# Kernel optimization log

Hardware: AMD Instinct MI355X
Metric: run time of the kernel (lower is better)

## Reference

```python
import jax, jax.numpy as jnp
import numpy as np
import math

B, T, C, H, D = 2, 2048, 768, 12, 64


def _rms_norm(x):
    # torch F.rms_norm with eps=None -> finfo(dtype).eps, no learned weight
    eps = jnp.finfo(x.dtype).eps
    return x * jax.lax.rsqrt(jnp.mean(x * x, axis=-1, keepdims=True) + eps)


def _apply_rotary(x, cos, sin):
    # nanochat rotary: split head_dim into halves
    d = x.shape[-1] // 2
    x1, x2 = x[..., :d], x[..., d:]
    return jnp.concatenate([x1 * cos + x2 * sin, -x1 * sin + x2 * cos], axis=-1)


def setup_inputs() -> dict:
    key = jax.random.key(0)
    ks = jax.random.split(key, 8)
    s = 0.02
    x = jax.random.normal(ks[0], (B, T, C), jnp.float32)
    cos = jax.random.normal(ks[1], (1, T, 1, D // 2), jnp.float32)
    sin = jax.random.normal(ks[2], (1, T, 1, D // 2), jnp.float32)
    Wq = jax.random.normal(ks[3], (C, C), jnp.float32) * s
    Wk = jax.random.normal(ks[4], (C, C), jnp.float32) * s
    Wv = jax.random.normal(ks[5], (C, C), jnp.float32) * s
    Wo = jax.random.normal(ks[6], (C, C), jnp.float32) * s
    beta = jnp.ones((H,), jnp.float32) * 0.5
    return {"x": x, "cos": cos, "sin": sin, "Wq": Wq, "Wk": Wk, "Wv": Wv, "Wo": Wo, "beta": beta}


def reference(x, cos, sin, Wq, Wk, Wv, Wo, beta):
    b, t, c = x.shape
    h = beta.shape[0]
    d = c // h
    q = (x @ Wq.T).reshape(b, t, h, d)
    k = (x @ Wk.T).reshape(b, t, h, d)
    v = (x @ Wv.T).reshape(b, t, h, d)
    q = _rms_norm(_apply_rotary(q, cos, sin)).transpose(0, 2, 1, 3)  # (B,H,T,D)
    k = _rms_norm(_apply_rotary(k, cos, sin)).transpose(0, 2, 1, 3)
    v = v.transpose(0, 2, 1, 3)
    # phase coherence: mean over RoPE frequencies of cos(position_diff * theta)
    pos = jnp.arange(t, dtype=jnp.float32)
    theta = 10000.0 ** (-jnp.arange(0, d, 2, dtype=jnp.float32) / d)  # (D/2,)
    pdiff = pos[None, :] - pos[:, None]  # (T,T); cos is even so orientation is irrelevant
    coh_base = jnp.mean(jnp.cos(pdiff[:, :, None] * theta), axis=-1)  # (T,T)
    coherence = 1.0 + beta[None, :, None, None] * coh_base[None, None, :, :]  # (1,H,T,T)
    scores = jnp.einsum('bhqd,bhkd->bhqk', q, k) / math.sqrt(d)
    scores = scores * coherence
    w = jax.nn.softmax(scores, axis=-1)
    causal = jnp.tril(jnp.ones((t, t), dtype=bool))
    w = w * causal[None, None, :, :]
    w = w / (jnp.sum(w, axis=-1, keepdims=True) + 1e-8)
    y = jnp.einsum('bhqk,bhkd->bhqd', w, v)
    y = y.transpose(0, 2, 1, 3).reshape(b, t, c)
    return y @ Wo.T
```

## Files before the change

kernel.cpp:

```cpp
#include <hip/hip_runtime.h>
#include <hip/hip_bf16.h>
#include <math.h>

#define B_ 2
#define T_ 2048
#define C_ 768
#define H_ 12
#define D_ 64

typedef __attribute__((ext_vector_type(8))) short short8;
typedef __attribute__((ext_vector_type(4))) float f32x4;
typedef __attribute__((ext_vector_type(16))) float f32x16;

template <bool V> struct BoolC { static constexpr bool value = V; };

#define SBAR() do { asm volatile("" ::: "memory"); __builtin_amdgcn_s_barrier(); asm volatile("" ::: "memory"); } while (0)
#define WAITVM(N) asm volatile("s_waitcnt vmcnt(" #N ")" ::: "memory")

__device__ inline unsigned short f2bf(float f) {
    unsigned int x = __float_as_uint(f);
    unsigned int r = x + 0x7FFFu + ((x >> 16) & 1u);
    return (unsigned short)(r >> 16);
}

__device__ __forceinline__ unsigned cvtpk(float lo, float hi) {
    unsigned r;
    asm("v_cvt_pk_bf16_f32 %0, %1, %2" : "=v"(r) : "v"(lo), "v"(hi));
    return r;
}

__device__ __forceinline__ void plswap(unsigned& a, unsigned& b) {
    asm volatile("v_permlane32_swap_b32 %0, %1" : "+v"(a), "+v"(b));
}

__device__ __forceinline__ void gll16(const void* g, void* l) {
    __builtin_amdgcn_global_load_lds(
        (const __attribute__((address_space(1))) unsigned int*)g,
        (__attribute__((address_space(3))) unsigned int*)l, 16, 0, 0);
}

__global__ __launch_bounds__(256) void convert_all_kernel(const float* __restrict__ x,
                                                          const float* __restrict__ Wq,
                                                          const float* __restrict__ Wk,
                                                          const float* __restrict__ Wv,
                                                          const float* __restrict__ Wo,
                                                          unsigned short* __restrict__ xb,
                                                          unsigned short* __restrict__ wqkv,
                                                          unsigned short* __restrict__ wob,
                                                          float* __restrict__ coh) {
    if (blockIdx.x >= 5376) {
        int dd = (blockIdx.x - 5376) * 256 + threadIdx.x;
        if (dd < T_) {
            float s = 0.f;
            for (int m = 0; m < 32; ++m) {
                float theta = powf(10000.f, -(float)m / 32.f);
                s += cosf((float)dd * theta);
            }
            coh[dd] = s * (1.f / 32.f);
        }
        return;
    }
    int i = blockIdx.x * 256 + threadIdx.x;
    float4 v;
    ushort4* d;
    if (i < 786432) {
        v = ((const float4*)x)[i];
        d = (ushort4*)xb + i;
    } else {
        int wI = i - 786432;
        int widx = wI / 147456;
        int off = wI - widx * 147456;
        const float* W = widx == 0 ? Wq : widx == 1 ? Wk : widx == 2 ? Wv : Wo;
        v = ((const float4*)W)[off];
        unsigned short* base = (widx == 3) ? wob : (wqkv + widx * 589824);
        d = (ushort4*)base + off;
    }
    ushort4 o;
    o.x = f2bf(v.x); o.y = f2bf(v.y); o.z = f2bf(v.z); o.w = f2bf(v.w);
    *d = o;
}

union QkvSmem {
    struct { unsigned short A[3][128][32]; unsigned short Bm[3][64][32]; } g;
    unsigned short tr[64][136];
};

__global__ __launch_bounds__(256, 4) void gemm_qkv_kernel(const unsigned short* __restrict__ xb,
                                                          const unsigned short* __restrict__ wqkv,
                                                          const float* __restrict__ cosb,
                                                          const float* __restrict__ sinb,
                                                          unsigned short* __restrict__ qbf,
                                                          unsigned short* __restrict__ kbf,
                                                          unsigned short* __restrict__ vt) {
    __shared__ QkvSmem sm;

    int bm = blockIdx.x, tn = blockIdx.y;
    int tid = threadIdx.x;
    int w = tid >> 6, lane = tid & 63;
    int rc = lane & 15, kg = lane >> 4;

    const unsigned short* ga = xb + (size_t)(bm * 128 + w * 32 + (lane >> 2)) * 768 + (lane & 3) * 8;
    const unsigned short* gb = wqkv + (size_t)(tn * 64 + w * 16 + (lane >> 2)) * 768 + (lane & 3) * 8;

    f32x4 acc[2][4];
    #pragma unroll
    for (int i = 0; i < 2; ++i)
        #pragma unroll
        for (int j = 0; j < 4; ++j) acc[i][j] = (f32x4){0.f, 0.f, 0.f, 0.f};

    auto stageg = [&](int buf, int k0) {
        gll16(ga + k0, &sm.g.A[buf][w * 32][0]);
        gll16(ga + k0 + 16 * 768, &sm.g.A[buf][w * 32 + 16][0]);
        gll16(gb + k0, &sm.g.Bm[buf][w * 16][0]);
    };
    auto comp = [&](int buf) {
        short8 aF[2], bF[4];
        #pragma unroll
        for (int ai = 0; ai < 2; ++ai) aF[ai] = *(const short8*)&sm.g.A[buf][w * 32 + ai * 16 + rc][kg * 8];
        #pragma unroll
        for (int bj = 0; bj < 4; ++bj) bF[bj] = *(const short8*)&sm.g.Bm[buf][bj * 16 + rc][kg * 8];
        __builtin_amdgcn_s_setprio(1);
        #pragma unroll
        for (int ai = 0; ai < 2; ++ai)
            #pragma unroll
            for (int bj = 0; bj < 4; ++bj)
                acc[ai][bj] = __builtin_amdgcn_mfma_f32_16x16x32_bf16(aF[ai], bF[bj], acc[ai][bj], 0, 0, 0);
        __builtin_amdgcn_s_setprio(0);
    };

    stageg(0, 0);
    stageg(1, 32);
    __syncthreads();
    for (int kk = 0; kk < 22; ++kk) {
        stageg((kk + 2) % 3, (kk + 2) * 32);
        WAITVM(6);
        SBAR();
        comp(kk % 3);
        SBAR();
    }
    WAITVM(3);
    SBAR();
    comp(1);
    SBAR();
    WAITVM(0);
    SBAR();
    comp(2);
    __syncthreads();

    int tensor = tn / 12;
    int h = tn % 12;

    if (tensor < 2) {
        float scale = tensor == 0 ? 0.125f : 1.0f;
        unsigned short* dst = (tensor == 0 ? qbf : kbf);
        #pragma unroll
        for (int ai = 0; ai < 2; ++ai) {
            #pragma unroll
            for (int rr = 0; rr < 4; ++rr) {
                int m = bm * 128 + w * 32 + ai * 16 + kg * 4 + rr;
                int b = m >> 11, t = m & 2047;
                float c0 = cosb[t * 32 + rc], c1 = cosb[t * 32 + 16 + rc];
                float s0 = sinb[t * 32 + rc], s1 = sinb[t * 32 + 16 + rc];
                float x0 = acc[ai][0][rr], x1 = acc[ai][1][rr];
                float x2 = acc[ai][2][rr], x3 = acc[ai][3][rr];
                float o0 = x0 * c0 + x2 * s0;
                float o1 = x1 * c1 + x3 * s1;
                float o2 = -x0 * s0 + x2 * c0;
                float o3 = -x1 * s1 + x3 * c1;
                float ss = o0 * o0 + o1 * o1 + o2 * o2 + o3 * o3;
                ss += __shfl_xor(ss, 1); ss += __shfl_xor(ss, 2);
                ss += __shfl_xor(ss, 4); ss += __shfl_xor(ss, 8);
                float rn = rsqrtf(ss * (1.f / 64.f) + 1.1920929e-07f) * scale;
                unsigned short* dp = dst + (((size_t)b * H_ + h) * T_ + t) * 64;
                dp[rc]      = f2bf(o0 * rn);
                dp[16 + rc] = f2bf(o1 * rn);
                dp[32 + rc] = f2bf(o2 * rn);
                dp[48 + rc] = f2bf(o3 * rn);
            }
        }
    } else {
        #pragma unroll
        for (int ai = 0; ai < 2; ++ai)
            #pragma unroll
            for (int bj = 0; bj < 4; ++bj)
                #pragma unroll
                for (int rr = 0; rr < 4; ++rr)
                    sm.tr[bj * 16 + rc][w * 32 + ai * 16 + kg * 4 + rr] = f2bf(acc[ai][bj][rr]);
        __syncthreads();
        int m0 = bm * 128;
        int b = m0 >> 11, t0 = m0 & 2047;
        int d = w * 16 + (lane >> 2);
        int tl = (lane & 3) * 32;
        unsigned short* gp = vt + (((size_t)b * H_ + h) * 64 + d) * T_ + t0 + tl;
        #pragma unroll
        for (int i = 0; i < 4; ++i)
            *(uint4*)(gp + i * 8) = *(const uint4*)&sm.tr[d][tl + i * 8];
    }
}

__global__ __launch_bounds__(256, 4) void gemm_out_kernel(const unsigned short* __restrict__ A,
                                                          const unsigned short* __restrict__ Bw,
                                                          float* __restrict__ C) {
    __shared__ unsigned short lA[2][64][32];
    __shared__ unsigned short lB[2][64][32];
    int bm = blockIdx.x, tn = blockIdx.y;
    int tid = threadIdx.x;
    int w = tid >> 6, lane = tid & 63;
    int rc = lane & 15, kg = lane >> 4;
    int wr = w >> 1, wc = w & 1;

    const unsigned short* ga = A + (size_t)(bm * 64 + w * 16 + (lane >> 2)) * 768 + (lane & 3) * 8;
    const unsigned short* gbB = Bw + (size_t)(tn * 64 + w * 16 + (lane >> 2)) * 768 + (lane & 3) * 8;

    f32x4 acc[2][2];
    #pragma unroll
    for (int i = 0; i < 2; ++i)
        #pragma unroll
        for (int j = 0; j < 2; ++j) acc[i][j] = (f32x4){0.f, 0.f, 0.f, 0.f};

    auto stageg = [&](int buf, int k0) {
        gll16(ga + k0, &lA[buf][w * 16][0]);
        gll16(gbB + k0, &lB[buf][w * 16][0]);
    };
    auto comp = [&](int buf) {
        short8 aF[2], bF[2];
        #pragma unroll
        for (int ai = 0; ai < 2; ++ai) aF[ai] = *(const short8*)&lA[buf][wr * 32 + ai * 16 + rc][kg * 8];
        #pragma unroll
        for (int bj = 0; bj < 2; ++bj) bF[bj] = *(const short8*)&lB[buf][wc * 32 + bj * 16 + rc][kg * 8];
        __builtin_amdgcn_s_setprio(1);
        #pragma unroll
        for (int ai = 0; ai < 2; ++ai)
            #pragma unroll
            for (int bj = 0; bj < 2; ++bj)
                acc[ai][bj] = __builtin_amdgcn_mfma_f32_16x16x32_bf16(aF[ai], bF[bj], acc[ai][bj], 0, 0, 0);
        __builtin_amdgcn_s_setprio(0);
    };

    stageg(0, 0);
    __syncthreads();
    for (int kk = 0; kk < 23; ++kk) {
        stageg((kk + 1) & 1, (kk + 1) * 32);
        WAITVM(2);
        SBAR();
        comp(kk & 1);
        SBAR();
    }
    WAITVM(0);
    SBAR();
    comp(1);

    #pragma unroll
    for (int ai = 0; ai < 2; ++ai)
        #pragma unroll
        for (int rr = 0; rr < 4; ++rr) {
            int m = bm * 64 + wr * 32 + ai * 16 + kg * 4 + rr;
            #pragma unroll
            for (int bj = 0; bj < 2; ++bj)
                C[(size_t)m * 768 + tn * 64 + wc * 32 + bj * 16 + rc] = acc[ai][bj][rr];
        }
}

__global__ __launch_bounds__(256, 4) void attn_flash_kernel(const unsigned short* __restrict__ qbf,
                                                            const unsigned short* __restrict__ kbf,
                                                            const unsigned short* __restrict__ vt,
                                                            const float* __restrict__ coh,
                                                            const float* __restrict__ beta,
                                                            unsigned short* __restrict__ yb) {
    __shared__ unsigned short kT[2][64][64];
    __shared__ unsigned short vT[2][64][64];
    __shared__ float cfl[T_];

    int p = blockIdx.x;
    int xcd = p & 7, kk = p >> 3;
    int bl = kk >> 5, c = kk & 31;
    int bh = xcd * 3 + bl;
    int tq;
    if (bl == 0)      tq = c;
    else if (bl == 1) tq = (c & 1) ? (15 - (c >> 1)) : (31 - (c >> 1));
    else              tq = (c & 1) ? (31 - (c >> 1)) : (15 - (c >> 1));
    int b = bh / H_, h = bh % H_;

    int tid = threadIdx.x;
    int w = tid >> 6, lane = tid & 63;
    int qs = w >> 1, js = w & 1;
    int ql = lane & 31, hl = lane >> 5;

    float bv = beta[h];
    int cmax4 = (tq + 1) * 16;
    for (int i = tid; i < cmax4; i += 256) {
        float4 cv = ((const float4*)coh)[i];
        float4 o;
        o.x = (1.f + bv * cv.x) * 1.4426950408889634f;
        o.y = (1.f + bv * cv.y) * 1.4426950408889634f;
        o.z = (1.f + bv * cv.z) * 1.4426950408889634f;
        o.w = (1.f + bv * cv.w) * 1.4426950408889634f;
        *(float4*)&cfl[i * 4] = o;
    }

    int qb = tq * 64;
    const unsigned short* kb = kbf + (size_t)bh * T_ * 64;
    const unsigned short* vb = vt + (size_t)bh * 64 * T_;

    const unsigned short* qrow = qbf + ((size_t)bh * T_ + qb + qs * 32 + ql) * 64 + hl * 8;
    short8 qf[4];
    #pragma unroll
    for (int d = 0; d < 4; ++d) qf[d] = *(const short8*)(qrow + d * 16);

    f32x16 acc0, acc1;
    #pragma unroll
    for (int i = 0; i < 16; ++i) { acc0[i] = 0.f; acc1[i] = 0.f; }
    float z = 0.f;

    int Rk = js * 32 + ql;
    int kby[4];
    #pragma unroll
    for (int d = 0; d < 4; ++d) kby[d] = Rk * 128 + (((d * 2 + hl) ^ (Rk & 7)) << 4);
    int vby0[2], vby1[2];
    #pragma unroll
    for (int ks = 0; ks < 2; ++ks) {
        int Rv0 = ql, Rv1 = 32 + ql;
        vby0[ks] = Rv0 * 128 + (((js * 4 + ks * 2 + hl) ^ (Rv0 & 7)) << 4);
        vby1[ks] = Rv1 * 128 + (((js * 4 + ks * 2 + hl) ^ (Rv1 & 7)) << 4);
    }
    const char* kbase = (const char*)&kT[0][0][0];
    const char* vbase = (const char*)&vT[0][0][0];

    int rloc = lane >> 3;
    int gsw = ((lane & 7) ^ rloc) * 8;
    int r0 = w * 16;

    auto stage = [&](int buf, int tj) {
        gll16(kb + (size_t)(tj + r0 + rloc) * 64 + gsw,      &kT[buf][r0][0]);
        gll16(kb + (size_t)(tj + r0 + 8 + rloc) * 64 + gsw,  &kT[buf][r0 + 8][0]);
        gll16(vb + (size_t)(r0 + rloc) * T_ + tj + gsw,      &vT[buf][r0][0]);
        gll16(vb + (size_t)(r0 + 8 + rloc) * T_ + tj + gsw,  &vT[buf][r0 + 8][0]);
    };

    int qpos = qb + qs * 32 + ql;

    auto body = [&](int buf, int tj, auto maskc) {
        constexpr bool M = decltype(maskc)::value;
        f32x16 s;
        #pragma unroll
        for (int i = 0; i < 16; ++i) s[i] = 0.f;
        const char* kp = kbase + buf * 8192;
        __builtin_amdgcn_s_setprio(1);
        #pragma unroll
        for (int d = 0; d < 4; ++d) {
            short8 kf = *(const short8*)(kp + kby[d]);
            s = __builtin_amdgcn_mfma_f32_32x32x16_bf16(kf, qf[d], s, 0, 0, 0);
        }
        __builtin_amdgcn_s_setprio(0);
        int base = qpos - tj - js * 32 - 4 * hl;
        float e[16];
        #pragma unroll
        for (int r = 0; r < 16; ++r) {
            int dd = base - ((r & 3) + 8 * (r >> 2));
            if constexpr (M) {
                float ex = __builtin_amdgcn_exp2f(s[r] * cfl[dd < 0 ? 0 : dd]);
                e[r] = dd >= 0 ? ex : 0.f;
            } else {
                e[r] = __builtin_amdgcn_exp2f(s[r] * cfl[dd]);
            }
            z += e[r];
        }
        unsigned A0 = cvtpk(e[0], e[1]),  B0 = cvtpk(e[2], e[3]);
        unsigned C0 = cvtpk(e[4], e[5]),  D0 = cvtpk(e[6], e[7]);
        unsigned E0 = cvtpk(e[8], e[9]),  F0 = cvtpk(e[10], e[11]);
        unsigned G0 = cvtpk(e[12], e[13]), H0 = cvtpk(e[14], e[15]);
        plswap(A0, C0); plswap(B0, D0); plswap(E0, G0); plswap(F0, H0);
        union U { unsigned u[4]; short8 s8; };
        U p0, p1;
        p0.u[0] = A0; p0.u[1] = B0; p0.u[2] = C0; p0.u[3] = D0;
        p1.u[0] = E0; p1.u[1] = F0; p1.u[2] = G0; p1.u[3] = H0;
        const char* vp = vbase + buf * 8192;
        short8 v00 = *(const short8*)(vp + vby0[0]);
        short8 v01 = *(const short8*)(vp + vby0[1]);
        short8 v10 = *(const short8*)(vp + vby1[0]);
        short8 v11 = *(const short8*)(vp + vby1[1]);
        __builtin_amdgcn_s_setprio(1);
        acc0 = __builtin_amdgcn_mfma_f32_32x32x16_bf16(v00, p0.s8, acc0, 0, 0, 0);
        acc0 = __builtin_amdgcn_mfma_f32_32x32x16_bf16(v01, p1.s8, acc0, 0, 0, 0);
        acc1 = __builtin_amdgcn_mfma_f32_32x32x16_bf16(v10, p0.s8, acc1, 0, 0, 0);
        acc1 = __builtin_amdgcn_mfma_f32_32x32x16_bf16(v11, p1.s8, acc1, 0, 0, 0);
        __builtin_amdgcn_s_setprio(0);
    };

    int nt = tq + 1;
    stage(0, 0);
    __syncthreads();
    int cur = 0;
    for (int it = 0; it < nt - 1; ++it) {
        stage(cur ^ 1, (it + 1) * 64);
        WAITVM(4);
        SBAR();
        body(cur, it * 64, BoolC<false>{});
        SBAR();
        cur ^= 1;
    }
    WAITVM(0);
    SBAR();
    if (qs > js)      body(cur, (nt - 1) * 64, BoolC<false>{});
    else if (qs == js) body(cur, (nt - 1) * 64, BoolC<true>{});
    __syncthreads();

    z += __shfl_xor(z, 32);
    float* osc = (float*)&kT[0][0][0];
    float* zbuf = (float*)&vT[0][0][0];
    if (js == 0) {
        float* o = osc + qs * 2048;
        #pragma unroll
        for (int r = 0; r < 16; ++r) {
            o[r * 64 + lane] = acc0[r];
            o[(16 + r) * 64 + lane] = acc1[r];
        }
        if (lane < 32) zbuf[qs * 32 + ql] = z;
    }
    __syncthreads();
    if (js == 1) {
        float zt = z + zbuf[qs * 32 + ql];
        float invz = 1.f / zt;
        const float* o = osc + qs * 2048;
        #pragma unroll
        for (int r = 0; r < 16; ++r) {
            acc0[r] = (acc0[r] + o[r * 64 + lane]) * invz;
            acc1[r] = (acc1[r] + o[(16 + r) * 64 + lane]) * invz;
        }
        int t = qb + qs * 32 + ql;
        unsigned short* yp = yb + (((size_t)b * T_ + t) * H_ + h) * 64;
        #pragma unroll
        for (int g = 0; g < 4; ++g) {
            uint2 st0, st1;
            st0.x = cvtpk(acc0[g * 4 + 0], acc0[g * 4 + 1]);
            st0.y = cvtpk(acc0[g * 4 + 2], acc0[g * 4 + 3]);
            *(uint2*)(yp + g * 8 + 4 * hl) = st0;
            st1.x = cvtpk(acc1[g * 4 + 0], acc1[g * 4 + 1]);
            st1.y = cvtpk(acc1[g * 4 + 2], acc1[g * 4 + 3]);
            *(uint2*)(yp + 32 + g * 8 + 4 * hl) = st1;
        }
    }
}

extern "C" void kernel_launch(void* const* d_in, const int* in_sizes, int n_in,
                              void* d_out, int out_size, void* d_ws, size_t ws_size,
                              hipStream_t stream) {
    const float* x    = (const float*)d_in[0];
    const float* cosb = (const float*)d_in[1];
    const float* sinb = (const float*)d_in[2];
    const float* Wq   = (const float*)d_in[3];
    const float* Wk   = (const float*)d_in[4];
    const float* Wv   = (const float*)d_in[5];
    const float* Wo   = (const float*)d_in[6];
    const float* beta = (const float*)d_in[7];
    float* out = (float*)d_out;

    char* ws = (char*)d_ws;
    unsigned short* xb   = (unsigned short*)(ws + 0);
    unsigned short* wqkv = (unsigned short*)(ws + 6291456);
    unsigned short* wob  = (unsigned short*)(ws + 9830400);
    unsigned short* qbf  = (unsigned short*)(ws + 11010048);
    unsigned short* kbf  = (unsigned short*)(ws + 17301504);
    unsigned short* vt   = (unsigned short*)(ws + 23592960);
    unsigned short* yb   = (unsigned short*)(ws + 29884416);
    float*          coh  = (float*)(ws + 36175872);

    convert_all_kernel<<<5384, 256, 0, stream>>>(x, Wq, Wk, Wv, Wo, xb, wqkv, wob, coh);

    dim3 gq(32, 36);
    gemm_qkv_kernel<<<gq, 256, 0, stream>>>(xb, wqkv, cosb, sinb, qbf, kbf, vt);

    attn_flash_kernel<<<B_ * H_ * (T_ / 64), 256, 0, stream>>>(qbf, kbf, vt, coh, beta, yb);

    dim3 go(64, 12);
    gemm_out_kernel<<<go, 256, 0, stream>>>(yb, wob, out);
}
```

Measured before the change: 97.64 us.

## Split long causal query tiles across two KV-range blocks with combine kernel

Query tiles 16-31 now have their key range split into two halves, each handled by a separate block that writes unnormalized partial outputs and softmax denominators to workspace. A new combine kernel sums the partials, normalizes, and writes bf16 output. The grid grows from 768 to 1152 blocks to even out the causal work imbalance and shorten the critical path. The cost is an extra launch plus fp32 partial traffic through global memory, and the combine kernel writes scattered 2-byte stores.

```diff
diff --git a/kernel.cpp b/kernel.cpp
--- a/kernel.cpp
+++ b/kernel.cpp
@@ -266,19 +266,29 @@
                                                             const unsigned short* __restrict__ vt,
                                                             const float* __restrict__ coh,
                                                             const float* __restrict__ beta,
-                                                            unsigned short* __restrict__ yb) {
+                                                            unsigned short* __restrict__ yb,
+                                                            float* __restrict__ po,
+                                                            float* __restrict__ pz) {
     __shared__ unsigned short kT[2][64][64];
     __shared__ unsigned short vT[2][64][64];
     __shared__ float cfl[T_];
 
     int p = blockIdx.x;
     int xcd = p & 7, kk = p >> 3;
-    int bl = kk >> 5, c = kk & 31;
+    int bl = kk / 48, u = kk % 48;
     int bh = xcd * 3 + bl;
-    int tq;
-    if (bl == 0)      tq = c;
-    else if (bl == 1) tq = (c & 1) ? (15 - (c >> 1)) : (31 - (c >> 1));
-    else              tq = (c & 1) ? (31 - (c >> 1)) : (15 - (c >> 1));
+    int tq, ts, te, part;
+    if (u < 16) { tq = u; ts = 0; te = tq + 1; part = 0; }
+    else {
+        int idx = u - 16;
+        tq = 16 + (idx >> 1);
+        part = idx & 1;
+        int ht = (tq + 1) >> 1;
+        ts = part ? ht : 0;
+        te = part ? (tq + 1) : ht;
+    }
+    bool hasdiag = (te == tq + 1);
+    bool partial = (u >= 16);
     int b = bh / H_, h = bh % H_;
 
     int tid = threadIdx.x;
@@ -286,9 +296,13 @@
     int qs = w >> 1, js = w & 1;
     int ql = lane & 31, hl = lane >> 5;
 
+    int qb = tq * 64;
     float bv = beta[h];
-    int cmax4 = (tq + 1) * 16;
-    for (int i = tid; i < cmax4; i += 256) {
+    int f0 = qb - te * 64 + 1;
+    if (f0 < 0) f0 = 0;
+    f0 >>= 2;
+    int f1 = (qb + 63 - ts * 64) >> 2;
+    for (int i = f0 + tid; i <= f1; i += 256) {
         float4 cv = ((const float4*)coh)[i];
         float4 o;
         o.x = (1.f + bv * cv.x) * 1.4426950408889634f;
@@ -298,7 +312,6 @@
         *(float4*)&cfl[i * 4] = o;
     }
 
-    int qb = tq * 64;
     const unsigned short* kb = kbf + (size_t)bh * T_ * 64;
     const unsigned short* vb = vt + (size_t)bh * 64 * T_;
 
@@ -387,11 +400,10 @@
         __builtin_amdgcn_s_setprio(0);
     };
 
-    int nt = tq + 1;
-    stage(0, 0);
+    stage(0, ts * 64);
     __syncthreads();
     int cur = 0;
-    for (int it = 0; it < nt - 1; ++it) {
+    for (int it = ts; it < te - 1; ++it) {
         stage(cur ^ 1, (it + 1) * 64);
         WAITVM(4);
         SBAR();
@@ -401,8 +413,12 @@
     }
     WAITVM(0);
     SBAR();
-    if (qs > js)      body(cur, (nt - 1) * 64, BoolC<false>{});
-    else if (qs == js) body(cur, (nt - 1) * 64, BoolC<true>{});
+    if (hasdiag) {
+        if (qs > js)       body(cur, (te - 1) * 64, BoolC<false>{});
+        else if (qs == js) body(cur, (te - 1) * 64, BoolC<true>{});
+    } else {
+        body(cur, (te - 1) * 64, BoolC<false>{});
+    }
     __syncthreads();
 
     z += __shfl_xor(z, 32);
@@ -419,26 +435,61 @@
     }
     __syncthreads();
     if (js == 1) {
-        float zt = z + zbuf[qs * 32 + ql];
-        float invz = 1.f / zt;
+        float zsum = z + zbuf[qs * 32 + ql];
         const float* o = osc + qs * 2048;
-        #pragma unroll
-        for (int r = 0; r < 16; ++r) {
-            acc0[r] = (acc0[r] + o[r * 64 + lane]) * invz;
-            acc1[r] = (acc1[r] + o[(16 + r) * 64 + lane]) * invz;
-        }
-        int t = qb + qs * 32 + ql;
-        unsigned short* yp = yb + (((size_t)b * T_ + t) * H_ + h) * 64;
-        #pragma unroll
-        for (int g = 0; g < 4; ++g) {
-            uint2 st0, st1;
-            st0.x = cvtpk(acc0[g * 4 + 0], acc0[g * 4 + 1]);
-            st0.y = cvtpk(acc0[g * 4 + 2], acc0[g * 4 + 3]);
-            *(uint2*)(yp + g * 8 + 4 * hl) = st0;
-            st1.x = cvtpk(acc1[g * 4 + 0], acc1[g * 4 + 1]);
-            st1.y = cvtpk(acc1[g * 4 + 2], acc1[g * 4 + 3]);
-            *(uint2*)(yp + 32 + g * 8 + 4 * hl) = st1;
-        }
+        if (!partial) {
+            float invz = 1.f / zsum;
+            #pragma unroll
+            for (int r = 0; r < 16; ++r) {
+                acc0[r] = (acc0[r] + o[r * 64 + lane]) * invz;
+                acc1[r] = (acc1[r] + o[(16 + r) * 64 + lane]) * invz;
+            }
+            int t = qb + qs * 32 + ql;
+            unsigned short* yp = yb + (((size_t)b * T_ + t) * H_ + h) * 64;
+            #pragma unroll
+            for (int g = 0; g < 4; ++g) {
+                uint2 st0, st1;
+                st0.x = cvtpk(acc0[g * 4 + 0], acc0[g * 4 + 1]);
+                st0.y = cvtpk(acc0[g * 4 + 2], acc0[g * 4 + 3]);
+                *(uint2*)(yp + g * 8 + 4 * hl) = st0;
+                st1.x = cvtpk(acc1[g * 4 + 0], acc1[g * 4 + 1]);
+                st1.y = cvtpk(acc1[g * 4 + 2], acc1[g * 4 + 3]);
+                *(uint2*)(yp + 32 + g * 8 + 4 * hl) = st1;
+            }
+        } else {
+            int slot = (bh * 16 + (tq - 16)) * 2 + part;
+            float* pob = po + (size_t)slot * 4096 + qs * 2048;
+            #pragma unroll
+            for (int r = 0; r < 16; ++r) {
+                pob[r * 64 + lane] = acc0[r] + o[r * 64 + lane];
+                pob[(16 + r) * 64 + lane] = acc1[r] + o[(16 + r) * 64 + lane];
+            }
+            if (hl == 0) pz[slot * 64 + qs * 32 + ql] = zsum;
+        }
+    }
+}
+
+__global__ __launch_bounds__(256) void attn_combine_kernel(const float* __restrict__ po,
+                                                           const float* __restrict__ pz,
+                                                           unsigned short* __restrict__ yb) {
+    int cb = blockIdx.x;
+    int bh = cb >> 4;
+    int tq = 16 + (cb & 15);
+    int b = bh / H_, h = bh % H_;
+    const float* p0 = po + (size_t)cb * 8192;
+    const float* p1 = p0 + 4096;
+    const float* z0 = pz + (size_t)cb * 128;
+    const float* z1 = z0 + 64;
+    for (int e = threadIdx.x; e < 4096; e += 256) {
+        int qs = e >> 11, r = (e >> 6) & 31, lane = e & 63;
+        int ql = lane & 31, hl = lane >> 5;
+        int row = qs * 32 + ql;
+        float invz = 1.f / (z0[row] + z1[row]);
+        int rb = r & 15;
+        int d = ((r >> 4) << 5) + ((rb >> 2) << 3) + (hl << 2) + (rb & 3);
+        float val = (p0[e] + p1[e]) * invz;
+        int t = tq * 64 + row;
+        yb[(((size_t)b * T_ + t) * H_ + h) * 64 + d] = f2bf(val);
     }
 }
 
@@ -464,13 +515,16 @@
     unsigned short* vt   = (unsigned short*)(ws + 23592960);
     unsigned short* yb   = (unsigned short*)(ws + 29884416);
     float*          coh  = (float*)(ws + 36175872);
+    float*          po   = (float*)(ws + 36184064);
+    float*          pz   = (float*)(ws + 48766976);
 
     convert_all_kernel<<<5384, 256, 0, stream>>>(x, Wq, Wk, Wv, Wo, xb, wqkv, wob, coh);
 
     dim3 gq(32, 36);
     gemm_qkv_kernel<<<gq, 256, 0, stream>>>(xb, wqkv, cosb, sinb, qbf, kbf, vt);
 
-    attn_flash_kernel<<<B_ * H_ * (T_ / 64), 256, 0, stream>>>(qbf, kbf, vt, coh, beta, yb);
+    attn_flash_kernel<<<1152, 256, 0, stream>>>(qbf, kbf, vt, coh, beta, yb, po, pz);
+    attn_combine_kernel<<<384, 256, 0, stream>>>(po, pz, yb);
 
     dim3 go(64, 12);
     gemm_out_kernel<<<go, 256, 0, stream>>>(yb, wob, out);
```

After: 106.7 us. 9.2% more time.
